# Optimization experiments

Hardware: AMD Instinct MI355X
Metric: run time of the kernel (lower is better)

The kernel has to match this reference:

```python
import jax, jax.numpy as jnp
import numpy as np

S, Q, N, T, G = 20000, 32, 200000, 30, 64
D_IN, H, D_SV, D_LANG, D_FUSE = 300, 256, 64, 64, 128

def setup_inputs() -> dict:
    key = jax.random.key(0)
    ks = jax.random.split(key, 20)
    sc = 0.05
    inp = {
        'lang_feat': jax.random.normal(ks[0], (Q, T, D_IN), jnp.float32),
        'supvox_feat': jax.random.normal(ks[1], (S, D_SV), jnp.float32),
        'supvox_coords': jax.random.uniform(ks[2], (S, 3), jnp.float32),
        'lang_len': jax.random.randint(ks[3], (Q,), 5, T + 1).astype(jnp.int32),
        'grps': jax.random.randint(ks[4], (S,), 0, G).astype(jnp.int32),
        'supervox': jax.random.randint(ks[5], (N,), 0, S).astype(jnp.int32),
        'gt': jax.random.randint(ks[6], (N, Q), 0, 2).astype(jnp.int32),
        # GRU params (torch layout: [3H, in])
        'gru_w_ih': sc * jax.random.normal(ks[7], (3 * H, D_IN), jnp.float32),
        'gru_w_hh': sc * jax.random.normal(ks[8], (3 * H, H), jnp.float32),
        'gru_b_ih': sc * jax.random.normal(ks[9], (3 * H,), jnp.float32),
        'gru_b_hh': sc * jax.random.normal(ks[10], (3 * H,), jnp.float32),
        # lang_sqz: Linear(256,64) ReLU Linear(64,64)
        'sqz_w1': sc * jax.random.normal(ks[11], (D_LANG, H), jnp.float32),
        'sqz_b1': sc * jax.random.normal(ks[12], (D_LANG,), jnp.float32),
        'sqz_w2': sc * jax.random.normal(ks[13], (D_LANG, D_LANG), jnp.float32),
        'sqz_b2': sc * jax.random.normal(ks[14], (D_LANG,), jnp.float32),
        # feat_fuse: Linear(131,128) ReLU
        'fuse_w': sc * jax.random.normal(ks[15], (D_FUSE, D_SV + 3 + D_LANG), jnp.float32),
        'fuse_b': sc * jax.random.normal(ks[16], (D_FUSE,), jnp.float32),
        # heat_map: Linear(128,2) (Dropout = identity in eval)
        'heat_w': sc * jax.random.normal(ks[17], (2, D_FUSE), jnp.float32),
        'heat_b': sc * jax.random.normal(ks[18], (2,), jnp.float32),
    }
    return inp

def _gru_last(x, lens, w_ih, w_hh, b_ih, b_hh):
    # x: [Q, T, D_IN]; returns hidden at step lens[q]-1 (pack_padded_sequence semantics)
    def step(h, xt_t):
        xt, t = xt_t  # xt: [Q, D_IN]
        gi = xt @ w_ih.T + b_ih          # [Q, 3H]
        gh = h @ w_hh.T + b_hh           # [Q, 3H]
        ir, iz, inn = jnp.split(gi, 3, -1)
        hr, hz, hn = jnp.split(gh, 3, -1)
        r = jax.nn.sigmoid(ir + hr)
        z = jax.nn.sigmoid(iz + hz)
        n = jnp.tanh(inn + r * hn)
        h_new = (1.0 - z) * n + z * h
        h = jnp.where((t < lens)[:, None], h_new, h)
        return h, None
    h0 = jnp.zeros((x.shape[0], w_hh.shape[1]), x.dtype)
    hT, _ = jax.lax.scan(step, h0, (jnp.swapaxes(x, 0, 1), jnp.arange(x.shape[1])))
    return hT  # [Q, H]

def reference(lang_feat, supvox_feat, supvox_coords, lang_len, grps, supervox, gt,
              gru_w_ih, gru_w_hh, gru_b_ih, gru_b_hh,
              sqz_w1, sqz_b1, sqz_w2, sqz_b2, fuse_w, fuse_b, heat_w, heat_b):
    # language branch
    h = _gru_last(lang_feat, lang_len, gru_w_ih, gru_w_hh, gru_b_ih, gru_b_hh)  # [Q,H]
    lang = jax.nn.relu(h @ sqz_w1.T + sqz_b1) @ sqz_w2.T + sqz_b2               # [Q,64]
    # supervoxel branch: cat(feat, coords) -> [S,67]
    sv = jnp.concatenate([supvox_feat, supvox_coords], -1)
    # feat_fuse on cat(sv, lang): split the weight to avoid materializing [S,Q,131]
    d_sv = sv.shape[-1]
    sv_proj = sv @ fuse_w[:, :d_sv].T           # [S,128]
    lang_proj = lang @ fuse_w[:, d_sv:].T       # [Q,128]
    fused = jax.nn.relu(sv_proj[:, None, :] + lang_proj[None, :, :] + fuse_b)  # [S,Q,128]
    logits = fused @ heat_w.T + heat_b          # [S,Q,2]
    obj_score = jax.nn.softmax(logits, -1)[..., 1]  # [S,Q]
    # cluster-grouped mean score (grps_ one-hot; assumes unique(grps)==arange(G))
    grp_oh = (grps[:, None] == jnp.arange(G)).astype(obj_score.dtype)  # [S,G]
    grp_sum = jnp.einsum('sq,sg->qg', obj_score, grp_oh)               # [Q,G]
    sen_grp_score = grp_sum / grp_oh.sum(0)[None, :]                   # [Q,G]
    best = jnp.argmax(sen_grp_score, -1)        # [Q]
    supvox_sen = grp_oh[:, best]                # [S,Q] binary
    obj_pts = supvox_sen[supervox].astype(jnp.int32)  # [N,Q]
    inter = (obj_pts * gt).sum(0).astype(jnp.float32)
    union = jnp.bitwise_or(obj_pts, gt).sum(0).astype(jnp.float32)
    ious = inter / (union + 1e-5)               # [Q]
    return obj_pts, ious
```

## Files before the change

### kernel.cpp

```cpp
#include <hip/hip_runtime.h>
#include <hip/hip_bf16.h>
#include <math.h>

#define S_TOT 20000
#define Q_TOT 32
#define N_TOT 200000
#define T_MAX 30
#define G_TOT 64
#define D_IN 300
#define H_DIM 256
#define D_SV 64
#define D_LANG 64
#define D_FUSE 128
#define D_CAT 67
#define FW_LD 131
#define SCHUNK 32
#define NBLK3 (S_TOT / SCHUNK)
#define SENT64 0xFFFFFFFFFFFFFFFFull
#define PCHUNK 16
#define PTILES 40
#define TAIL_GRID 1024

#define GI_MT 32
#define GI_NT 64
#define GI_KC 100
#define GI_NB 12
#define GI_GRID (30 * GI_NB)
#define HG_ELEMS (30 * Q_TOT * H_DIM)

#define SYNCS_N 5376

__device__ __forceinline__ float sigmoidf_(float x) { return 1.0f / (1.0f + expf(-x)); }
__device__ __forceinline__ unsigned long long pack2(float a, float b) {
    return ((unsigned long long)__float_as_uint(b) << 32) | (unsigned long long)__float_as_uint(a);
}

__global__ __launch_bounds__(128) void k_gi(const float* __restrict__ lang_feat,
                                            const float* __restrict__ w_ih,
                                            const float* __restrict__ b_ih,
                                            const float* __restrict__ fuse_w,
                                            const float* __restrict__ sqz_w1,
                                            const float* __restrict__ sqz_w2,
                                            const float* __restrict__ heat_w,
                                            float* __restrict__ gi,
                                            float* __restrict__ fwt,
                                            float* __restrict__ w1t,
                                            float* __restrict__ w2t,
                                            float* __restrict__ wdr,
                                            float* __restrict__ hg,
                                            int* __restrict__ syncs) {
    const int tid = threadIdx.x;
    if (blockIdx.x >= GI_GRID) {
        const int xb = blockIdx.x - GI_GRID;
        if (xb == 0) {
            for (int i = tid; i < FW_LD * D_FUSE; i += 128)
                fwt[(i % FW_LD) * D_FUSE + (i / FW_LD)] = fuse_w[i];
            for (int i = tid; i < D_LANG * H_DIM; i += 128)
                w1t[(i & 255) * D_LANG + (i >> 8)] = sqz_w1[i];
            for (int i = tid; i < D_LANG * D_LANG; i += 128)
                w2t[(i & 63) * D_LANG + (i >> 6)] = sqz_w2[i];
            if (tid < D_FUSE) wdr[tid] = heat_w[D_FUSE + tid] - heat_w[tid];
        } else {
            const int fb = xb - 1;
            const int per4 = HG_ELEMS / 4 / 8;
            float4* dst = (float4*)hg + fb * per4;
            const float4 sv = make_float4(__uint_as_float(0xFFFFFFFFu), __uint_as_float(0xFFFFFFFFu),
                                          __uint_as_float(0xFFFFFFFFu), __uint_as_float(0xFFFFFFFFu));
            for (int i = tid; i < per4; i += 128) dst[i] = sv;
            if (fb == 0) for (int i = tid; i < SYNCS_N; i += 128) syncs[i] = 0;
        }
        return;
    }
    __shared__ float x_l[GI_KC][GI_MT + 1];
    __shared__ float w_l[GI_KC][GI_NT + 1];
    const int mb = blockIdx.x / GI_NB, nb = blockIdx.x % GI_NB;
    const int m0 = mb * GI_MT, n0 = nb * GI_NT;
    const int tq4 = (tid >> 4) * 4, jq4 = (tid & 15) * 4;

    float acc[4][4];
    #pragma unroll
    for (int i = 0; i < 4; ++i)
        #pragma unroll
        for (int j = 0; j < 4; ++j) acc[i][j] = 0.f;

    for (int kc = 0; kc < 3; ++kc) {
        const int k0 = kc * GI_KC;
        for (int i = tid; i < GI_MT * GI_KC; i += 128) {
            const int r = i / GI_KC, k = i % GI_KC;
            const int row = m0 + r, q = row / T_MAX, t = row - q * T_MAX;
            x_l[k][r] = lang_feat[(q * T_MAX + t) * D_IN + k0 + k];
        }
        for (int i = tid; i < GI_NT * GI_KC; i += 128) {
            const int r = i / GI_KC, k = i % GI_KC;
            w_l[k][r] = w_ih[(n0 + r) * D_IN + k0 + k];
        }
        __syncthreads();
        #pragma unroll 2
        for (int k = 0; k < GI_KC; ++k) {
            const float x0 = x_l[k][tq4 + 0], x1 = x_l[k][tq4 + 1];
            const float x2 = x_l[k][tq4 + 2], x3 = x_l[k][tq4 + 3];
            const float v0 = w_l[k][jq4 + 0], v1 = w_l[k][jq4 + 1];
            const float v2 = w_l[k][jq4 + 2], v3 = w_l[k][jq4 + 3];
            acc[0][0] = fmaf(x0, v0, acc[0][0]); acc[0][1] = fmaf(x0, v1, acc[0][1]);
            acc[0][2] = fmaf(x0, v2, acc[0][2]); acc[0][3] = fmaf(x0, v3, acc[0][3]);
            acc[1][0] = fmaf(x1, v0, acc[1][0]); acc[1][1] = fmaf(x1, v1, acc[1][1]);
            acc[1][2] = fmaf(x1, v2, acc[1][2]); acc[1][3] = fmaf(x1, v3, acc[1][3]);
            acc[2][0] = fmaf(x2, v0, acc[2][0]); acc[2][1] = fmaf(x2, v1, acc[2][1]);
            acc[2][2] = fmaf(x2, v2, acc[2][2]); acc[2][3] = fmaf(x2, v3, acc[2][3]);
            acc[3][0] = fmaf(x3, v0, acc[3][0]); acc[3][1] = fmaf(x3, v1, acc[3][1]);
            acc[3][2] = fmaf(x3, v2, acc[3][2]); acc[3][3] = fmaf(x3, v3, acc[3][3]);
        }
        __syncthreads();
    }
    const float b0 = b_ih[n0 + jq4 + 0], b1 = b_ih[n0 + jq4 + 1];
    const float b2 = b_ih[n0 + jq4 + 2], b3 = b_ih[n0 + jq4 + 3];
    #pragma unroll
    for (int i = 0; i < 4; ++i) {
        const int row = m0 + tq4 + i;
        const int q = row / T_MAX, t = row - q * T_MAX;
        float4 v = make_float4(acc[i][0] + b0, acc[i][1] + b1, acc[i][2] + b2, acc[i][3] + b3);
        *(float4*)&gi[(q * T_MAX + t) * 768 + n0 + jq4] = v;
    }
}

__global__ __launch_bounds__(384, 1) void k_gru8(const float* __restrict__ gi,
                                                 const float* __restrict__ w_hh,
                                                 const float* __restrict__ b_hh,
                                                 const int* __restrict__ lang_len,
                                                 float* __restrict__ hg,
                                                 float* __restrict__ hbuf,
                                                 const float* __restrict__ w1t,
                                                 const float* __restrict__ b1,
                                                 const float* __restrict__ w2t,
                                                 const float* __restrict__ b2,
                                                 const float* __restrict__ fwt,
                                                 const float* __restrict__ fuse_b,
                                                 float* __restrict__ langc,
                                                 int* __restrict__ qdone) {
    __shared__ __align__(16) float wlds[96 * 256];
    __shared__ __align__(16) float hlq[4 * 68];
    __shared__ float ghl[96];
    __shared__ float gil[T_MAX * 96];

    const int tid = threadIdx.x;
    const int q = blockIdx.x >> 3, b = blockIdx.x & 7;
    int len = lang_len[q]; if (len > T_MAX) len = T_MAX; if (len < 1) len = 1;

    {
        const float4* src4 = (const float4*)w_hh;
        float4* dst4 = (float4*)wlds;
        for (int i = tid; i < 96 * 64; i += 384) {
            const int r = i >> 6, c = i & 63;
            const int grow = ((r >> 5) << 8) + (b << 5) + (r & 31);
            dst4[r * 64 + (c ^ (r & 7))] = src4[grow * 64 + c];
        }
    }
    for (int i = tid; i < len * 96; i += 384) {
        const int t = i / 96, r = i % 96;
        gil[i] = gi[(q * T_MAX + t) * 768 + ((r >> 5) << 8) + (b << 5) + (r & 31)];
    }
    __syncthreads();

    float hfin = 0.f;
    {
        float hnew = 0.f;
        if (tid < 32) {
            const float bhr = b_hh[(b << 5) + tid];
            const float bhz = b_hh[H_DIM + (b << 5) + tid];
            const float bhn = b_hh[2 * H_DIM + (b << 5) + tid];
            const float r = sigmoidf_(gil[tid] + bhr);
            const float z = sigmoidf_(gil[32 + tid] + bhz);
            const float n = tanhf(gil[64 + tid] + r * bhn);
            hnew = (1.f - z) * n;
            if (len == 1) hfin = hnew;
        }
        if (tid < 64 && len > 1) {
            const float a0 = __shfl(hnew, 2 * (tid & 15));
            const float a1 = __shfl(hnew, 2 * (tid & 15) + 1);
            if (tid < 16) {
                unsigned long long* dst = (unsigned long long*)(hg + q * H_DIM + (b << 5));
                __hip_atomic_store(dst + tid, pack2(a0, a1), __ATOMIC_RELAXED, __HIP_MEMORY_SCOPE_AGENT);
            }
        }
    }

    const int row = tid >> 2, ql = tid & 3;
    const float bh = b_hh[((row >> 5) << 8) + (b << 5) + (row & 31)];
    const int rx = row & 7;
    const float4* wrow4 = (const float4*)wlds + row * 64;
    const int cbase = ql << 4;

    for (int t = 1; t < len; ++t) {
        if (tid < 128) {
            const unsigned long long* src =
                (const unsigned long long*)(hg + (size_t)(t - 1) * (Q_TOT * H_DIM) + q * H_DIM);
            unsigned long long v;
            while ((v = __hip_atomic_load(src + tid, __ATOMIC_RELAXED,
                                          __HIP_MEMORY_SCOPE_AGENT)) == SENT64)
                __builtin_amdgcn_s_sleep(1);
            const int k = 2 * tid;
            const int o = (k >> 6) * 68 + (k & 63);
            hlq[o]     = __uint_as_float((unsigned)(v & 0xffffffffu));
            hlq[o + 1] = __uint_as_float((unsigned)(v >> 32));
        }
        __syncthreads();
        float hold = 0.f;
        if (tid < 32) { const int k = (b << 5) + tid; hold = hlq[(k >> 6) * 68 + (k & 63)]; }
        const float4* h4 = (const float4*)(hlq + ql * 68);
        float ax = 0.f, ay = 0.f, az = 0.f, aw = 0.f;
        #pragma unroll
        for (int i = 0; i < 16; ++i) {
            const float4 wv = wrow4[(cbase + i) ^ rx];
            const float4 hv = h4[i];
            ax = fmaf(wv.x, hv.x, ax);
            ay = fmaf(wv.y, hv.y, ay);
            az = fmaf(wv.z, hv.z, az);
            aw = fmaf(wv.w, hv.w, aw);
        }
        float s = (ax + ay) + (az + aw);
        s += __shfl_xor(s, 1);
        s += __shfl_xor(s, 2);
        if (ql == 0) ghl[row] = s + bh;
        __syncthreads();
        float hnew = 0.f;
        if (tid < 32) {
            const float* gt_ = gil + t * 96;
            const float r = sigmoidf_(gt_[tid] + ghl[tid]);
            const float z = sigmoidf_(gt_[32 + tid] + ghl[32 + tid]);
            const float n = tanhf(gt_[64 + tid] + r * ghl[64 + tid]);
            hnew = (1.f - z) * n + z * hold;
            if (t == len - 1) hfin = hnew;
        }
        if (tid < 64 && t < len - 1) {
            const float a0 = __shfl(hnew, 2 * (tid & 15));
            const float a1 = __shfl(hnew, 2 * (tid & 15) + 1);
            if (tid < 16) {
                unsigned long long* dst =
                    (unsigned long long*)(hg + (size_t)t * (Q_TOT * H_DIM) + q * H_DIM + (b << 5));
                __hip_atomic_store(dst + tid, pack2(a0, a1), __ATOMIC_RELAXED, __HIP_MEMORY_SCOPE_AGENT);
            }
        }
    }

    if (tid < 32)
        __hip_atomic_store(&hbuf[q * H_DIM + (b << 5) + tid], hfin,
                           __ATOMIC_RELAXED, __HIP_MEMORY_SCOPE_AGENT);
    asm volatile("s_waitcnt vmcnt(0)" ::: "memory");
    __syncthreads();
    if (tid == 0)
        __hip_atomic_fetch_add(&qdone[32 * q], 1, __ATOMIC_RELAXED, __HIP_MEMORY_SCOPE_AGENT);
    if (b != 0) return;

    if (tid == 0) {
        while (__hip_atomic_load(&qdone[32 * q], __ATOMIC_RELAXED, __HIP_MEMORY_SCOPE_AGENT) < 8)
            __builtin_amdgcn_s_sleep(2);
    }
    __syncthreads();
    float* hql = gil;
    float* t1l = gil + 256;
    float* lgl = gil + 320;
    if (tid < H_DIM)
        hql[tid] = __hip_atomic_load(&hbuf[q * H_DIM + tid], __ATOMIC_RELAXED, __HIP_MEMORY_SCOPE_AGENT);
    __syncthreads();
    if (tid < 256) {
        const int c = tid >> 2, qq = tid & 3;
        float a = 0.f;
        #pragma unroll 8
        for (int j = 0; j < 64; ++j) {
            const int k = (qq << 6) + j;
            a = fmaf(w1t[k * D_LANG + c], hql[k], a);
        }
        a += __shfl_xor(a, 1);
        a += __shfl_xor(a, 2);
        if (qq == 0) t1l[c] = fmaxf(a + b1[c], 0.f);
    }
    __syncthreads();
    if (tid < 256) {
        const int c = tid >> 2, qq = tid & 3;
        float a = 0.f;
        #pragma unroll
        for (int j = 0; j < 16; ++j) {
            const int k = (qq << 4) + j;
            a = fmaf(w2t[k * D_LANG + c], t1l[k], a);
        }
        a += __shfl_xor(a, 1);
        a += __shfl_xor(a, 2);
        if (qq == 0) lgl[c] = a + b2[c];
    }
    __syncthreads();
    if (tid < 256) {
        const int d = tid >> 1, hh = tid & 1;
        float a = 0.f;
        #pragma unroll 8
        for (int j = 0; j < 32; ++j) {
            const int k = (hh << 5) + j;
            a = fmaf(fwt[(D_CAT + k) * D_FUSE + d], lgl[k], a);
        }
        a += __shfl_xor(a, 1);
        if (hh == 0) langc[q * D_FUSE + d] = a + fuse_b[d];
    }
}

__global__ __launch_bounds__(256, 3) void k_tail(const float* __restrict__ feat,
                                                 const float* __restrict__ coords,
                                                 const int* __restrict__ grps,
                                                 const float* __restrict__ langc,
                                                 const float* __restrict__ fwt,
                                                 const float* __restrict__ wdr_g,
                                                 const float* __restrict__ heat_b,
                                                 float* __restrict__ grp_part,
                                                 int* __restrict__ cnt_part,
                                                 float* __restrict__ grp2,
                                                 int* __restrict__ cnt2,
                                                 int* __restrict__ best,
                                                 const int* __restrict__ supervox,
                                                 const int* __restrict__ gt,
                                                 float* __restrict__ out,
                                                 int* __restrict__ syncs) {
    const int tid = threadIdx.x;
    const int bid = blockIdx.x;

    __shared__ __align__(16) float svin[SCHUNK][68];
    __shared__ __align__(16) float svp[SCHUNK][132];
    __shared__ float score[SCHUNK][Q_TOT];
    __shared__ int grps_l[SCHUNK];
    __shared__ float ps[4][G_TOT];
    __shared__ int   pc[4][G_TOT];
    __shared__ float sc[G_TOT];
    __shared__ int bl[Q_TOT];
    __shared__ int gm[G_TOT];
    __shared__ int bi_s[Q_TOT], bu_s[Q_TOT];
    __shared__ int islast;

    if (bid < NBLK3) {
        const int s0 = bid * SCHUNK;
        const int dsl = tid & 7, q = tid >> 3;
        float lc[16], wdr[16];
        #pragma unroll
        for (int i = 0; i < 16; ++i) {
            const int d = dsl * 16 + i;
            lc[i]  = langc[q * D_FUSE + d];
            wdr[i] = wdr_g[d];
        }
        const float hbd = heat_b[1] - heat_b[0];

        for (int i = tid; i < SCHUNK * D_SV; i += 256) {
            const int r = i >> 6, c = i & 63;
            svin[r][c] = feat[(s0 + r) * D_SV + c];
        }
        if (tid < SCHUNK * 3) { const int r = tid / 3, c = tid % 3; svin[r][D_SV + c] = coords[(s0 + r) * 3 + c]; }
        if (tid < SCHUNK) grps_l[tid] = grps[s0 + tid];
        __syncthreads();

        {
            const int d = tid & 127, sl0 = tid >> 7;
            float acc[16];
            #pragma unroll
            for (int i = 0; i < 16; ++i) acc[i] = 0.f;
            for (int k4 = 0; k4 < 16; ++k4) {
                const float w0 = fwt[(4 * k4 + 0) * D_FUSE + d];
                const float w1 = fwt[(4 * k4 + 1) * D_FUSE + d];
                const float w2 = fwt[(4 * k4 + 2) * D_FUSE + d];
                const float w3 = fwt[(4 * k4 + 3) * D_FUSE + d];
                #pragma unroll
                for (int i = 0; i < 16; ++i) {
                    const float4 xv = *(const float4*)&svin[sl0 + 2 * i][4 * k4];
                    acc[i] = fmaf(xv.x, w0, fmaf(xv.y, w1, fmaf(xv.z, w2, fmaf(xv.w, w3, acc[i]))));
                }
            }
            for (int k = 64; k < D_CAT; ++k) {
                const float wv = fwt[k * D_FUSE + d];
                #pragma unroll
                for (int i = 0; i < 16; ++i)
                    acc[i] = fmaf(svin[sl0 + 2 * i][k], wv, acc[i]);
            }
            #pragma unroll
            for (int i = 0; i < 16; ++i) svp[sl0 + 2 * i][d] = acc[i];
        }
        __syncthreads();

        for (int sl = 0; sl < SCHUNK; ++sl) {
            const float4* sv4 = (const float4*)(&svp[sl][dsl * 16]);
            float part = 0.f;
            #pragma unroll
            for (int j = 0; j < 4; ++j) {
                const float4 v = sv4[j];
                part = fmaf(fmaxf(v.x + lc[4*j+0], 0.f), wdr[4*j+0], part);
                part = fmaf(fmaxf(v.y + lc[4*j+1], 0.f), wdr[4*j+1], part);
                part = fmaf(fmaxf(v.z + lc[4*j+2], 0.f), wdr[4*j+2], part);
                part = fmaf(fmaxf(v.w + lc[4*j+3], 0.f), wdr[4*j+3], part);
            }
            part += __shfl_xor(part, 1);
            part += __shfl_xor(part, 2);
            part += __shfl_xor(part, 4);
            if (dsl == 0) score[sl][q] = sigmoidf_(part + hbd);
        }
        __syncthreads();

        for (int i = 0; i < 8; ++i) {
            const int cell = tid + 256 * i;
            const int qq = cell >> 6, g = cell & 63;
            float sum = 0.f;
            #pragma unroll
            for (int sl = 0; sl < SCHUNK; ++sl)
                sum += (grps_l[sl] == g) ? score[sl][qq] : 0.f;
            __hip_atomic_store(&grp_part[bid * (Q_TOT * G_TOT) + cell], sum,
                               __ATOMIC_RELAXED, __HIP_MEMORY_SCOPE_AGENT);
            if (cell < G_TOT) {
                int c = 0;
                #pragma unroll
                for (int sl = 0; sl < SCHUNK; ++sl) c += (grps_l[sl] == g);
                __hip_atomic_store(&cnt_part[bid * G_TOT + g], c,
                                   __ATOMIC_RELAXED, __HIP_MEMORY_SCOPE_AGENT);
            }
        }
        asm volatile("s_waitcnt vmcnt(0)" ::: "memory");
        __syncthreads();
        if (tid == 0)
            __hip_atomic_fetch_add(&syncs[4096 + 32 * (bid / PTILES)], 1,
                                   __ATOMIC_RELAXED, __HIP_MEMORY_SCOPE_AGENT);
    }

    if (bid < Q_TOT * PCHUNK) {
        const int q = bid & 31, c = bid >> 5;
        const int b0 = c * PTILES;
        int b1 = b0 + PTILES; if (b1 > NBLK3) b1 = NBLK3;
        if (tid == 0) {
            int* tc = &syncs[4096 + 32 * c];
            const int tgt = b1 - b0;
            while (__hip_atomic_load(tc, __ATOMIC_RELAXED, __HIP_MEMORY_SCOPE_AGENT) < tgt)
                __builtin_amdgcn_s_sleep(4);
        }
        __syncthreads();
        const int bq = tid >> 6, g = tid & 63;
        float acc = 0.f; int cacc = 0;
        for (int b = b0 + bq; b < b1; b += 4) {
            acc  += grp_part[b * (Q_TOT * G_TOT) + q * G_TOT + g];
            cacc += cnt_part[b * G_TOT + g];
        }
        ps[bq][g] = acc; pc[bq][g] = cacc;
        __syncthreads();
        if (tid < G_TOT) {
            const float s = ((ps[0][tid] + ps[1][tid]) + ps[2][tid]) + ps[3][tid];
            const int  cc = ((pc[0][tid] + pc[1][tid]) + pc[2][tid]) + pc[3][tid];
            __hip_atomic_store(&grp2[(c * Q_TOT + q) * G_TOT + tid], s,
                               __ATOMIC_RELAXED, __HIP_MEMORY_SCOPE_AGENT);
            __hip_atomic_store(&cnt2[(c * Q_TOT + q) * G_TOT + tid], cc,
                               __ATOMIC_RELAXED, __HIP_MEMORY_SCOPE_AGENT);
        }
        __shared__ int myturn;
        asm volatile("s_waitcnt vmcnt(0)" ::: "memory");
        if (tid == 0) {
            const int old = __hip_atomic_fetch_add(&syncs[3072 + 32 * q], 1,
                                                   __ATOMIC_RELAXED, __HIP_MEMORY_SCOPE_AGENT);
            myturn = (old == PCHUNK - 1) ? 1 : 0;
        }
        __syncthreads();
        if (myturn) {
            if (tid < G_TOT) {
                float s = 0.f; int cc = 0;
                #pragma unroll
                for (int c2 = 0; c2 < PCHUNK; ++c2) {
                    s  += grp2[(c2 * Q_TOT + q) * G_TOT + tid];
                    cc += cnt2[(c2 * Q_TOT + q) * G_TOT + tid];
                }
                sc[tid] = s / (float)cc;
            }
            __syncthreads();
            if (tid == 0) {
                float bv = sc[0]; int bi = 0;
                for (int g2 = 1; g2 < G_TOT; ++g2) if (sc[g2] > bv) { bv = sc[g2]; bi = g2; }
                __hip_atomic_store(&best[q], bi, __ATOMIC_RELAXED, __HIP_MEMORY_SCOPE_AGENT);
                asm volatile("s_waitcnt vmcnt(0)" ::: "memory");
                const int old = __hip_atomic_fetch_add(&syncs[5152 + 32], 1,
                                                       __ATOMIC_RELAXED, __HIP_MEMORY_SCOPE_AGENT);
                if (old == Q_TOT - 1) {
                    #pragma unroll
                    for (int f = 0; f < 8; ++f)
                        __hip_atomic_store(&syncs[4608 + 32 * f], 1,
                                           __ATOMIC_RELAXED, __HIP_MEMORY_SCOPE_AGENT);
                }
            }
        }
    }

    if (tid == 0) {
        int* fl = &syncs[4608 + 32 * (bid & 7)];
        while (__hip_atomic_load(fl, __ATOMIC_RELAXED, __HIP_MEMORY_SCOPE_AGENT) == 0)
            __builtin_amdgcn_s_sleep(16);
    }
    __syncthreads();

    if (tid < Q_TOT) bl[tid] = best[tid];
    __syncthreads();
    if (tid < G_TOT) {
        int m = 0;
        #pragma unroll
        for (int qq = 0; qq < Q_TOT; ++qq) m |= (bl[qq] == tid) ? (1 << qq) : 0;
        gm[tid] = m;
    }
    __syncthreads();

    {
        const int gidx = bid * 256 + tid;
        const int q4 = (gidx & 7) * 4;
        const int nstride = (TAIL_GRID * 256) >> 3;
        int a0 = 0, a1 = 0, a2 = 0, a3 = 0;
        int u0 = 0, u1 = 0, u2 = 0, u3 = 0;
        for (int n = gidx >> 3; n < N_TOT; n += nstride) {
            const int m = gm[grps[supervox[n]]];
            const int4 g4 = *(const int4*)&gt[n * Q_TOT + q4];
            const int o0 = (m >> (q4 + 0)) & 1;
            const int o1 = (m >> (q4 + 1)) & 1;
            const int o2 = (m >> (q4 + 2)) & 1;
            const int o3 = (m >> (q4 + 3)) & 1;
            *(float4*)&out[n * Q_TOT + q4] =
                make_float4((float)o0, (float)o1, (float)o2, (float)o3);
            a0 += o0 & g4.x; u0 += o0 | g4.x;
            a1 += o1 & g4.y; u1 += o1 | g4.y;
            a2 += o2 & g4.z; u2 += o2 | g4.z;
            a3 += o3 & g4.w; u3 += o3 | g4.w;
        }
        if (tid < Q_TOT) { bi_s[tid] = 0; bu_s[tid] = 0; }
        __syncthreads();
        atomicAdd(&bi_s[q4 + 0], a0); atomicAdd(&bu_s[q4 + 0], u0);
        atomicAdd(&bi_s[q4 + 1], a1); atomicAdd(&bu_s[q4 + 1], u1);
        atomicAdd(&bi_s[q4 + 2], a2); atomicAdd(&bu_s[q4 + 2], u2);
        atomicAdd(&bi_s[q4 + 3], a3); atomicAdd(&bu_s[q4 + 3], u3);
        __syncthreads();
        if (tid < Q_TOT) {
            atomicAdd(&syncs[32 * tid], bi_s[tid]);
            atomicAdd(&syncs[1024 + 32 * tid], bu_s[tid]);
        }
        asm volatile("s_waitcnt vmcnt(0)" ::: "memory");
        if (tid == 0) {
            islast = 0;
            const int sub = bid & 7;
            const int o1_ = __hip_atomic_fetch_add(&syncs[4864 + 32 * sub], 1,
                                                   __ATOMIC_RELAXED, __HIP_MEMORY_SCOPE_AGENT);
            if (o1_ == (TAIL_GRID / 8) - 1) {
                const int o2_ = __hip_atomic_fetch_add(&syncs[5152], 1,
                                                       __ATOMIC_RELAXED, __HIP_MEMORY_SCOPE_AGENT);
                islast = (o2_ == 7) ? 1 : 0;
            }
        }
        __syncthreads();
        if (islast && tid < Q_TOT) {
            const int iv = __hip_atomic_load(&syncs[32 * tid], __ATOMIC_RELAXED, __HIP_MEMORY_SCOPE_AGENT);
            const int uv = __hip_atomic_load(&syncs[1024 + 32 * tid], __ATOMIC_RELAXED, __HIP_MEMORY_SCOPE_AGENT);
            out[(size_t)N_TOT * Q_TOT + tid] = (float)iv / ((float)uv + 1e-5f);
        }
    }
}

extern "C" void kernel_launch(void* const* d_in, const int* in_sizes, int n_in,
                              void* d_out, int out_size, void* d_ws, size_t ws_size,
                              hipStream_t stream) {
    const float* lang_feat = (const float*)d_in[0];
    const float* feat      = (const float*)d_in[1];
    const float* coords    = (const float*)d_in[2];
    const int*   lang_len  = (const int*)d_in[3];
    const int*   grps      = (const int*)d_in[4];
    const int*   supervox  = (const int*)d_in[5];
    const int*   gt        = (const int*)d_in[6];
    const float* w_ih      = (const float*)d_in[7];
    const float* w_hh      = (const float*)d_in[8];
    const float* b_ih      = (const float*)d_in[9];
    const float* b_hh      = (const float*)d_in[10];
    const float* sqz_w1    = (const float*)d_in[11];
    const float* sqz_b1    = (const float*)d_in[12];
    const float* sqz_w2    = (const float*)d_in[13];
    const float* sqz_b2    = (const float*)d_in[14];
    const float* fuse_w    = (const float*)d_in[15];
    const float* fuse_b    = (const float*)d_in[16];
    const float* heat_w    = (const float*)d_in[17];
    const float* heat_b    = (const float*)d_in[18];
    float* out = (float*)d_out;

    float* gi       = (float*)d_ws;
    float* hbuf     = gi + 737280;
    float* langc    = hbuf + 8192;
    float* grp_part = langc + 4096;
    int*   cnt_part = (int*)(grp_part + NBLK3 * 2048);
    int*   best     = cnt_part + NBLK3 * 64;
    int*   syncs    = best + 32;
    float* hg       = (float*)(syncs + SYNCS_N);
    float* fwt      = hg + HG_ELEMS;
    float* w1t      = fwt + FW_LD * D_FUSE;
    float* w2t      = w1t + H_DIM * D_LANG;
    float* wdr      = w2t + D_LANG * D_LANG;
    float* grp2     = wdr + 128;
    int*   cnt2     = (int*)(grp2 + PCHUNK * Q_TOT * G_TOT);

    k_gi   <<<GI_GRID + 9, 128, 0, stream>>>(lang_feat, w_ih, b_ih, fuse_w, sqz_w1, sqz_w2, heat_w,
                                             gi, fwt, w1t, w2t, wdr, hg, syncs);
    k_gru8 <<<Q_TOT * 8, 384, 0, stream>>>(gi, w_hh, b_hh, lang_len, hg, hbuf,
                                           w1t, sqz_b1, w2t, sqz_b2, fwt, fuse_b, langc,
                                           syncs + 2048);
    k_tail <<<TAIL_GRID, 256, 0, stream>>>(feat, coords, grps, langc, fwt, wdr, heat_b,
                                           grp_part, cnt_part, grp2, cnt2, best,
                                           supervox, gt, out, syncs);
}
```

Baseline: 203.6 us.

## Split tail kernel into fuse and output kernels, replacing spin-wait barrier

The fused tail kernel, which used a grid-wide spin-wait flag between the scoring/argmax phase and the output/IoU phase, is split into two launches. k_fuseA runs only the score blocks (NBLK3 of them) and k_out2 runs the output pass with a larger grid. This removes the in-kernel spin barrier and the idle blocks waiting on it, at the cost of an extra kernel launch and losing overlap of output-phase setup with the tail of the fuse phase.

```diff
diff --git a/kernel.cpp b/kernel.cpp
--- a/kernel.cpp
+++ b/kernel.cpp
@@ -19,7 +19,7 @@
 #define SENT64 0xFFFFFFFFFFFFFFFFull
 #define PCHUNK 16
 #define PTILES 40
-#define TAIL_GRID 1024
+#define OUT_GRID 2048
 
 #define GI_MT 32
 #define GI_NT 64
@@ -301,22 +301,19 @@
     }
 }
 
-__global__ __launch_bounds__(256, 3) void k_tail(const float* __restrict__ feat,
-                                                 const float* __restrict__ coords,
-                                                 const int* __restrict__ grps,
-                                                 const float* __restrict__ langc,
-                                                 const float* __restrict__ fwt,
-                                                 const float* __restrict__ wdr_g,
-                                                 const float* __restrict__ heat_b,
-                                                 float* __restrict__ grp_part,
-                                                 int* __restrict__ cnt_part,
-                                                 float* __restrict__ grp2,
-                                                 int* __restrict__ cnt2,
-                                                 int* __restrict__ best,
-                                                 const int* __restrict__ supervox,
-                                                 const int* __restrict__ gt,
-                                                 float* __restrict__ out,
-                                                 int* __restrict__ syncs) {
+__global__ __launch_bounds__(256, 3) void k_fuseA(const float* __restrict__ feat,
+                                                  const float* __restrict__ coords,
+                                                  const int* __restrict__ grps,
+                                                  const float* __restrict__ langc,
+                                                  const float* __restrict__ fwt,
+                                                  const float* __restrict__ wdr_g,
+                                                  const float* __restrict__ heat_b,
+                                                  float* __restrict__ grp_part,
+                                                  int* __restrict__ cnt_part,
+                                                  float* __restrict__ grp2,
+                                                  int* __restrict__ cnt2,
+                                                  int* __restrict__ best,
+                                                  int* __restrict__ syncs) {
     const int tid = threadIdx.x;
     const int bid = blockIdx.x;
 
@@ -327,12 +324,8 @@
     __shared__ float ps[4][G_TOT];
     __shared__ int   pc[4][G_TOT];
     __shared__ float sc[G_TOT];
-    __shared__ int bl[Q_TOT];
-    __shared__ int gm[G_TOT];
-    __shared__ int bi_s[Q_TOT], bu_s[Q_TOT];
-    __shared__ int islast;
-
-    if (bid < NBLK3) {
+
+    {
         const int s0 = bid * SCHUNK;
         const int dsl = tid & 7, q = tid >> 3;
         float lc[16], wdr[16];
@@ -471,25 +464,23 @@
                 float bv = sc[0]; int bi = 0;
                 for (int g2 = 1; g2 < G_TOT; ++g2) if (sc[g2] > bv) { bv = sc[g2]; bi = g2; }
                 __hip_atomic_store(&best[q], bi, __ATOMIC_RELAXED, __HIP_MEMORY_SCOPE_AGENT);
-                asm volatile("s_waitcnt vmcnt(0)" ::: "memory");
-                const int old = __hip_atomic_fetch_add(&syncs[5152 + 32], 1,
-                                                       __ATOMIC_RELAXED, __HIP_MEMORY_SCOPE_AGENT);
-                if (old == Q_TOT - 1) {
-                    #pragma unroll
-                    for (int f = 0; f < 8; ++f)
-                        __hip_atomic_store(&syncs[4608 + 32 * f], 1,
-                                           __ATOMIC_RELAXED, __HIP_MEMORY_SCOPE_AGENT);
-                }
-            }
-        }
-    }
-
-    if (tid == 0) {
-        int* fl = &syncs[4608 + 32 * (bid & 7)];
-        while (__hip_atomic_load(fl, __ATOMIC_RELAXED, __HIP_MEMORY_SCOPE_AGENT) == 0)
-            __builtin_amdgcn_s_sleep(16);
-    }
-    __syncthreads();
+            }
+        }
+    }
+}
+
+__global__ __launch_bounds__(256) void k_out2(const int* __restrict__ grps,
+                                              const int* __restrict__ best,
+                                              const int* __restrict__ supervox,
+                                              const int* __restrict__ gt,
+                                              float* __restrict__ out,
+                                              int* __restrict__ syncs) {
+    const int tid = threadIdx.x;
+    const int bid = blockIdx.x;
+    __shared__ int bl[Q_TOT];
+    __shared__ int gm[G_TOT];
+    __shared__ int bi_s[Q_TOT], bu_s[Q_TOT];
+    __shared__ int islast;
 
     if (tid < Q_TOT) bl[tid] = best[tid];
     __syncthreads();
@@ -499,57 +490,54 @@
         for (int qq = 0; qq < Q_TOT; ++qq) m |= (bl[qq] == tid) ? (1 << qq) : 0;
         gm[tid] = m;
     }
-    __syncthreads();
-
-    {
-        const int gidx = bid * 256 + tid;
-        const int q4 = (gidx & 7) * 4;
-        const int nstride = (TAIL_GRID * 256) >> 3;
-        int a0 = 0, a1 = 0, a2 = 0, a3 = 0;
-        int u0 = 0, u1 = 0, u2 = 0, u3 = 0;
-        for (int n = gidx >> 3; n < N_TOT; n += nstride) {
-            const int m = gm[grps[supervox[n]]];
-            const int4 g4 = *(const int4*)&gt[n * Q_TOT + q4];
-            const int o0 = (m >> (q4 + 0)) & 1;
-            const int o1 = (m >> (q4 + 1)) & 1;
-            const int o2 = (m >> (q4 + 2)) & 1;
-            const int o3 = (m >> (q4 + 3)) & 1;
-            *(float4*)&out[n * Q_TOT + q4] =
-                make_float4((float)o0, (float)o1, (float)o2, (float)o3);
-            a0 += o0 & g4.x; u0 += o0 | g4.x;
-            a1 += o1 & g4.y; u1 += o1 | g4.y;
-            a2 += o2 & g4.z; u2 += o2 | g4.z;
-            a3 += o3 & g4.w; u3 += o3 | g4.w;
-        }
-        if (tid < Q_TOT) { bi_s[tid] = 0; bu_s[tid] = 0; }
-        __syncthreads();
-        atomicAdd(&bi_s[q4 + 0], a0); atomicAdd(&bu_s[q4 + 0], u0);
-        atomicAdd(&bi_s[q4 + 1], a1); atomicAdd(&bu_s[q4 + 1], u1);
-        atomicAdd(&bi_s[q4 + 2], a2); atomicAdd(&bu_s[q4 + 2], u2);
-        atomicAdd(&bi_s[q4 + 3], a3); atomicAdd(&bu_s[q4 + 3], u3);
-        __syncthreads();
-        if (tid < Q_TOT) {
-            atomicAdd(&syncs[32 * tid], bi_s[tid]);
-            atomicAdd(&syncs[1024 + 32 * tid], bu_s[tid]);
-        }
-        asm volatile("s_waitcnt vmcnt(0)" ::: "memory");
-        if (tid == 0) {
-            islast = 0;
-            const int sub = bid & 7;
-            const int o1_ = __hip_atomic_fetch_add(&syncs[4864 + 32 * sub], 1,
+    if (tid < Q_TOT) { bi_s[tid] = 0; bu_s[tid] = 0; }
+    __syncthreads();
+
+    const int gidx = bid * 256 + tid;
+    const int q4 = (gidx & 7) * 4;
+    const int nstride = (OUT_GRID * 256) >> 3;
+    int a0 = 0, a1 = 0, a2 = 0, a3 = 0;
+    int u0 = 0, u1 = 0, u2 = 0, u3 = 0;
+    for (int n = gidx >> 3; n < N_TOT; n += nstride) {
+        const int m = gm[grps[supervox[n]]];
+        const int4 g4 = *(const int4*)&gt[n * Q_TOT + q4];
+        const int o0 = (m >> (q4 + 0)) & 1;
+        const int o1 = (m >> (q4 + 1)) & 1;
+        const int o2 = (m >> (q4 + 2)) & 1;
+        const int o3 = (m >> (q4 + 3)) & 1;
+        *(float4*)&out[n * Q_TOT + q4] =
+            make_float4((float)o0, (float)o1, (float)o2, (float)o3);
+        a0 += o0 & g4.x; u0 += o0 | g4.x;
+        a1 += o1 & g4.y; u1 += o1 | g4.y;
+        a2 += o2 & g4.z; u2 += o2 | g4.z;
+        a3 += o3 & g4.w; u3 += o3 | g4.w;
+    }
+    atomicAdd(&bi_s[q4 + 0], a0); atomicAdd(&bu_s[q4 + 0], u0);
+    atomicAdd(&bi_s[q4 + 1], a1); atomicAdd(&bu_s[q4 + 1], u1);
+    atomicAdd(&bi_s[q4 + 2], a2); atomicAdd(&bu_s[q4 + 2], u2);
+    atomicAdd(&bi_s[q4 + 3], a3); atomicAdd(&bu_s[q4 + 3], u3);
+    __syncthreads();
+    if (tid < Q_TOT) {
+        atomicAdd(&syncs[32 * tid], bi_s[tid]);
+        atomicAdd(&syncs[1024 + 32 * tid], bu_s[tid]);
+    }
+    asm volatile("s_waitcnt vmcnt(0)" ::: "memory");
+    if (tid == 0) {
+        islast = 0;
+        const int sub = bid & 7;
+        const int o1_ = __hip_atomic_fetch_add(&syncs[4864 + 32 * sub], 1,
+                                               __ATOMIC_RELAXED, __HIP_MEMORY_SCOPE_AGENT);
+        if (o1_ == (OUT_GRID / 8) - 1) {
+            const int o2_ = __hip_atomic_fetch_add(&syncs[5152], 1,
                                                    __ATOMIC_RELAXED, __HIP_MEMORY_SCOPE_AGENT);
-            if (o1_ == (TAIL_GRID / 8) - 1) {
-                const int o2_ = __hip_atomic_fetch_add(&syncs[5152], 1,
-                                                       __ATOMIC_RELAXED, __HIP_MEMORY_SCOPE_AGENT);
-                islast = (o2_ == 7) ? 1 : 0;
-            }
-        }
-        __syncthreads();
-        if (islast && tid < Q_TOT) {
-            const int iv = __hip_atomic_load(&syncs[32 * tid], __ATOMIC_RELAXED, __HIP_MEMORY_SCOPE_AGENT);
-            const int uv = __hip_atomic_load(&syncs[1024 + 32 * tid], __ATOMIC_RELAXED, __HIP_MEMORY_SCOPE_AGENT);
-            out[(size_t)N_TOT * Q_TOT + tid] = (float)iv / ((float)uv + 1e-5f);
-        }
+            islast = (o2_ == 7) ? 1 : 0;
+        }
+    }
+    __syncthreads();
+    if (islast && tid < Q_TOT) {
+        const int iv = __hip_atomic_load(&syncs[32 * tid], __ATOMIC_RELAXED, __HIP_MEMORY_SCOPE_AGENT);
+        const int uv = __hip_atomic_load(&syncs[1024 + 32 * tid], __ATOMIC_RELAXED, __HIP_MEMORY_SCOPE_AGENT);
+        out[(size_t)N_TOT * Q_TOT + tid] = (float)iv / ((float)uv + 1e-5f);
     }
 }
 
@@ -592,12 +580,12 @@
     float* grp2     = wdr + 128;
     int*   cnt2     = (int*)(grp2 + PCHUNK * Q_TOT * G_TOT);
 
-    k_gi   <<<GI_GRID + 9, 128, 0, stream>>>(lang_feat, w_ih, b_ih, fuse_w, sqz_w1, sqz_w2, heat_w,
-                                             gi, fwt, w1t, w2t, wdr, hg, syncs);
-    k_gru8 <<<Q_TOT * 8, 384, 0, stream>>>(gi, w_hh, b_hh, lang_len, hg, hbuf,
-                                           w1t, sqz_b1, w2t, sqz_b2, fwt, fuse_b, langc,
-                                           syncs + 2048);
-    k_tail <<<TAIL_GRID, 256, 0, stream>>>(feat, coords, grps, langc, fwt, wdr, heat_b,
-                                           grp_part, cnt_part, grp2, cnt2, best,
-                                           supervox, gt, out, syncs);
+    k_gi    <<<GI_GRID + 9, 128, 0, stream>>>(lang_feat, w_ih, b_ih, fuse_w, sqz_w1, sqz_w2, heat_w,
+                                              gi, fwt, w1t, w2t, wdr, hg, syncs);
+    k_gru8  <<<Q_TOT * 8, 384, 0, stream>>>(gi, w_hh, b_hh, lang_len, hg, hbuf,
+                                            w1t, sqz_b1, w2t, sqz_b2, fwt, fuse_b, langc,
+                                            syncs + 2048);
+    k_fuseA <<<NBLK3, 256, 0, stream>>>(feat, coords, grps, langc, fwt, wdr, heat_b,
+                                        grp_part, cnt_part, grp2, cnt2, best, syncs);
+    k_out2  <<<OUT_GRID, 256, 0, stream>>>(grps, best, supervox, gt, out, syncs);
 }
```

After: 212.5 us. 4.4% more time.

## Replace sentinel-polled hidden-state exchange with per-step counter flags; shrink tail grid

Applied to the files above, without the earlier changes.

The GRU kernel no longer fills the whole hidden-state exchange buffer with sentinel values and spins on every 64-bit word. Each of the eight blocks per query now bumps a per-step flag counter after its hidden-state store, and readers wait until the counter reaches eight before loading. This removes the large sentinel-fill pass in the first kernel and replaces many polling loads with a single flag poll, at the cost of an extra waitcnt and atomic per step. The tail kernel grid also shrinks from 1024 to NBLK3 (625) blocks, so every block runs the scoring phase; the last-block detection targets are adjusted to match.

```diff
diff --git a/kernel.cpp b/kernel.cpp
--- a/kernel.cpp
+++ b/kernel.cpp
@@ -16,10 +16,8 @@
 #define FW_LD 131
 #define SCHUNK 32
 #define NBLK3 (S_TOT / SCHUNK)
-#define SENT64 0xFFFFFFFFFFFFFFFFull
 #define PCHUNK 16
 #define PTILES 40
-#define TAIL_GRID 1024
 
 #define GI_MT 32
 #define GI_NT 64
@@ -27,6 +25,7 @@
 #define GI_NB 12
 #define GI_GRID (30 * GI_NB)
 #define HG_ELEMS (30 * Q_TOT * H_DIM)
+#define HFLAG_N (Q_TOT * T_MAX * 32)
 
 #define SYNCS_N 5376
 
@@ -47,7 +46,7 @@
                                             float* __restrict__ w1t,
                                             float* __restrict__ w2t,
                                             float* __restrict__ wdr,
-                                            float* __restrict__ hg,
+                                            int* __restrict__ hflag,
                                             int* __restrict__ syncs) {
     const int tid = threadIdx.x;
     if (blockIdx.x >= GI_GRID) {
@@ -62,11 +61,8 @@
             if (tid < D_FUSE) wdr[tid] = heat_w[D_FUSE + tid] - heat_w[tid];
         } else {
             const int fb = xb - 1;
-            const int per4 = HG_ELEMS / 4 / 8;
-            float4* dst = (float4*)hg + fb * per4;
-            const float4 sv = make_float4(__uint_as_float(0xFFFFFFFFu), __uint_as_float(0xFFFFFFFFu),
-                                          __uint_as_float(0xFFFFFFFFu), __uint_as_float(0xFFFFFFFFu));
-            for (int i = tid; i < per4; i += 128) dst[i] = sv;
+            const int per = HFLAG_N / 8;
+            for (int i = tid; i < per; i += 128) hflag[fb * per + i] = 0;
             if (fb == 0) for (int i = tid; i < SYNCS_N; i += 128) syncs[i] = 0;
         }
         return;
@@ -136,6 +132,7 @@
                                                  const float* __restrict__ fwt,
                                                  const float* __restrict__ fuse_b,
                                                  float* __restrict__ langc,
+                                                 int* __restrict__ hflag,
                                                  int* __restrict__ qdone) {
     __shared__ __align__(16) float wlds[96 * 256];
     __shared__ __align__(16) float hlq[4 * 68];
@@ -182,6 +179,12 @@
                 __hip_atomic_store(dst + tid, pack2(a0, a1), __ATOMIC_RELAXED, __HIP_MEMORY_SCOPE_AGENT);
             }
         }
+        if (len > 1) {
+            asm volatile("s_waitcnt vmcnt(0)" ::: "memory");
+            if (tid == 0)
+                __hip_atomic_fetch_add(&hflag[(q * T_MAX + 0) * 32], 1,
+                                       __ATOMIC_RELAXED, __HIP_MEMORY_SCOPE_AGENT);
+        }
     }
 
     const int row = tid >> 2, ql = tid & 3;
@@ -192,12 +195,13 @@
 
     for (int t = 1; t < len; ++t) {
         if (tid < 128) {
+            const int fidx = (q * T_MAX + (t - 1)) * 32;
+            while (__hip_atomic_load(&hflag[fidx], __ATOMIC_RELAXED, __HIP_MEMORY_SCOPE_AGENT) < 8)
+                __builtin_amdgcn_s_sleep(1);
             const unsigned long long* src =
                 (const unsigned long long*)(hg + (size_t)(t - 1) * (Q_TOT * H_DIM) + q * H_DIM);
-            unsigned long long v;
-            while ((v = __hip_atomic_load(src + tid, __ATOMIC_RELAXED,
-                                          __HIP_MEMORY_SCOPE_AGENT)) == SENT64)
-                __builtin_amdgcn_s_sleep(1);
+            const unsigned long long v =
+                __hip_atomic_load(src + tid, __ATOMIC_RELAXED, __HIP_MEMORY_SCOPE_AGENT);
             const int k = 2 * tid;
             const int o = (k >> 6) * 68 + (k & 63);
             hlq[o]     = __uint_as_float((unsigned)(v & 0xffffffffu));
@@ -231,14 +235,20 @@
             hnew = (1.f - z) * n + z * hold;
             if (t == len - 1) hfin = hnew;
         }
-        if (tid < 64 && t < len - 1) {
-            const float a0 = __shfl(hnew, 2 * (tid & 15));
-            const float a1 = __shfl(hnew, 2 * (tid & 15) + 1);
-            if (tid < 16) {
-                unsigned long long* dst =
-                    (unsigned long long*)(hg + (size_t)t * (Q_TOT * H_DIM) + q * H_DIM + (b << 5));
-                __hip_atomic_store(dst + tid, pack2(a0, a1), __ATOMIC_RELAXED, __HIP_MEMORY_SCOPE_AGENT);
-            }
+        if (t < len - 1) {
+            if (tid < 64) {
+                const float a0 = __shfl(hnew, 2 * (tid & 15));
+                const float a1 = __shfl(hnew, 2 * (tid & 15) + 1);
+                if (tid < 16) {
+                    unsigned long long* dst =
+                        (unsigned long long*)(hg + (size_t)t * (Q_TOT * H_DIM) + q * H_DIM + (b << 5));
+                    __hip_atomic_store(dst + tid, pack2(a0, a1), __ATOMIC_RELAXED, __HIP_MEMORY_SCOPE_AGENT);
+                }
+            }
+            asm volatile("s_waitcnt vmcnt(0)" ::: "memory");
+            if (tid == 0)
+                __hip_atomic_fetch_add(&hflag[(q * T_MAX + t) * 32], 1,
+                                       __ATOMIC_RELAXED, __HIP_MEMORY_SCOPE_AGENT);
         }
     }
 
@@ -332,7 +342,7 @@
     __shared__ int bi_s[Q_TOT], bu_s[Q_TOT];
     __shared__ int islast;
 
-    if (bid < NBLK3) {
+    {
         const int s0 = bid * SCHUNK;
         const int dsl = tid & 7, q = tid >> 3;
         float lc[16], wdr[16];
@@ -472,7 +482,7 @@
                 for (int g2 = 1; g2 < G_TOT; ++g2) if (sc[g2] > bv) { bv = sc[g2]; bi = g2; }
                 __hip_atomic_store(&best[q], bi, __ATOMIC_RELAXED, __HIP_MEMORY_SCOPE_AGENT);
                 asm volatile("s_waitcnt vmcnt(0)" ::: "memory");
-                const int old = __hip_atomic_fetch_add(&syncs[5152 + 32], 1,
+                const int old = __hip_atomic_fetch_add(&syncs[5184], 1,
                                                        __ATOMIC_RELAXED, __HIP_MEMORY_SCOPE_AGENT);
                 if (old == Q_TOT - 1) {
                     #pragma unroll
@@ -504,7 +514,7 @@
     {
         const int gidx = bid * 256 + tid;
         const int q4 = (gidx & 7) * 4;
-        const int nstride = (TAIL_GRID * 256) >> 3;
+        const int nstride = (NBLK3 * 256) >> 3;
         int a0 = 0, a1 = 0, a2 = 0, a3 = 0;
         int u0 = 0, u1 = 0, u2 = 0, u3 = 0;
         for (int n = gidx >> 3; n < N_TOT; n += nstride) {
@@ -536,9 +546,10 @@
         if (tid == 0) {
             islast = 0;
             const int sub = bid & 7;
+            const int subtgt = (sub == 0) ? 79 : 78;
             const int o1_ = __hip_atomic_fetch_add(&syncs[4864 + 32 * sub], 1,
                                                    __ATOMIC_RELAXED, __HIP_MEMORY_SCOPE_AGENT);
-            if (o1_ == (TAIL_GRID / 8) - 1) {
+            if (o1_ == subtgt - 1) {
                 const int o2_ = __hip_atomic_fetch_add(&syncs[5152], 1,
                                                        __ATOMIC_RELAXED, __HIP_MEMORY_SCOPE_AGENT);
                 islast = (o2_ == 7) ? 1 : 0;
@@ -584,7 +595,8 @@
     int*   cnt_part = (int*)(grp_part + NBLK3 * 2048);
     int*   best     = cnt_part + NBLK3 * 64;
     int*   syncs    = best + 32;
-    float* hg       = (float*)(syncs + SYNCS_N);
+    int*   hflag    = syncs + SYNCS_N;
+    float* hg       = (float*)(hflag + HFLAG_N);
     float* fwt      = hg + HG_ELEMS;
     float* w1t      = fwt + FW_LD * D_FUSE;
     float* w2t      = w1t + H_DIM * D_LANG;
@@ -593,11 +605,11 @@
     int*   cnt2     = (int*)(grp2 + PCHUNK * Q_TOT * G_TOT);
 
     k_gi   <<<GI_GRID + 9, 128, 0, stream>>>(lang_feat, w_ih, b_ih, fuse_w, sqz_w1, sqz_w2, heat_w,
-                                             gi, fwt, w1t, w2t, wdr, hg, syncs);
+                                             gi, fwt, w1t, w2t, wdr, hflag, syncs);
     k_gru8 <<<Q_TOT * 8, 384, 0, stream>>>(gi, w_hh, b_hh, lang_len, hg, hbuf,
                                            w1t, sqz_b1, w2t, sqz_b2, fwt, fuse_b, langc,
-                                           syncs + 2048);
-    k_tail <<<TAIL_GRID, 256, 0, stream>>>(feat, coords, grps, langc, fwt, wdr, heat_b,
-                                           grp_part, cnt_part, grp2, cnt2, best,
-                                           supervox, gt, out, syncs);
+                                           hflag, syncs + 2048);
+    k_tail <<<NBLK3, 256, 0, stream>>>(feat, coords, grps, langc, fwt, wdr, heat_b,
+                                       grp_part, cnt_part, grp2, cnt2, best,
+                                       supervox, gt, out, syncs);
 }
```

Measured after the change: 223.4 us. 1.1x slower.
